# Kernel optimization log

Measured on AMD Instinct MI355X. Metric: run time of the kernel, lower is better.

## Reference

```python
import jax, jax.numpy as jnp
import numpy as np

POS_THRESH = 0.5

def cxcy_to_xy(cxcy):
    return jnp.concatenate([cxcy[..., :2] - cxcy[..., 2:] / 2,
                            cxcy[..., :2] + cxcy[..., 2:] / 2], axis=-1)

def xy_to_cxcy(xy):
    return jnp.concatenate([(xy[..., :2] + xy[..., 2:]) / 2,
                            xy[..., 2:] - xy[..., :2]], axis=-1)

def iou_matrix(a, b):
    # a: [A,4] corner boxes, b: [N,4] corner boxes -> [A,N]
    lt = jnp.maximum(a[:, None, :2], b[None, :, :2])
    rb = jnp.minimum(a[:, None, 2:], b[None, :, 2:])
    wh = jnp.clip(rb - lt, 0.0)
    inter = wh[..., 0] * wh[..., 1]
    area_a = (a[:, 2] - a[:, 0]) * (a[:, 3] - a[:, 1])
    area_b = (b[:, 2] - b[:, 0]) * (b[:, 3] - b[:, 1])
    return inter / (area_a[:, None] + area_b[None, :] - inter)

def encode(gt_cxcy, anc_cxcy):
    # standard SSD variance encoding
    g_cxcy = (gt_cxcy[:, :2] - anc_cxcy[:, :2]) / (anc_cxcy[:, 2:] / 10.0)
    g_wh = jnp.log(gt_cxcy[:, 2:] / anc_cxcy[:, 2:]) * 5.0
    return jnp.concatenate([g_cxcy, g_wh], axis=1)

def setup_inputs() -> dict:
    key = jax.random.key(0)
    k1, k2, k3, k4, k5 = jax.random.split(key, 5)
    B, N, A = 64, 64, 24564
    # valid gt corner boxes in [0,1]
    gc = jax.random.uniform(k1, (B, N, 2), minval=0.2, maxval=0.8)
    gwh = jax.random.uniform(k2, (B, N, 2), minval=0.05, maxval=0.3)
    gt_boxes = jnp.concatenate([gc - gwh / 2, gc + gwh / 2], axis=-1)
    gt_labels = jax.random.randint(k3, (B, N), 0, 20)
    ac = jax.random.uniform(k4, (A, 2), minval=0.05, maxval=0.95)
    awh = jax.random.uniform(k5, (A, 2), minval=0.03, maxval=0.5)
    center_anchor = jnp.concatenate([ac, awh], axis=-1)
    return {"gt_boxes": gt_boxes, "gt_labels": gt_labels, "center_anchor": center_anchor}

def _match_one(boxes, labels, center_anchor, corner_anchor):
    # boxes:[N,4] corner, labels:[N], anchors:[A,4]
    N = boxes.shape[0]
    iou = iou_matrix(corner_anchor, boxes)            # [A,N]
    obj_idx = jnp.argmax(iou, axis=0)                 # best anchor per object [N]
    iou = iou.at[obj_idx, jnp.arange(N)].set(1.0)     # force-match
    positive = jnp.any(iou >= POS_THRESH, axis=1)     # [A] bool
    max_anchors_idx = jnp.argmax(iou, axis=1)         # best object per anchor [A]
    classes = (labels[max_anchors_idx] + 1) * positive.astype(labels.dtype)
    gt_center = xy_to_cxcy(boxes[max_anchors_idx])    # [A,4]
    locations = encode(gt_center, center_anchor)      # [A,4]
    return classes, locations, positive

def reference(gt_boxes, gt_labels, center_anchor):
    corner_anchor = cxcy_to_xy(center_anchor)
    gt_classes, gt_locations, gt_masks = jax.vmap(
        lambda b, l: _match_one(b, l, center_anchor, corner_anchor)
    )(gt_boxes, gt_labels)
    return gt_classes, gt_locations, gt_masks
```

## Files before the change

### kernel.cpp

```cpp
#include <hip/hip_runtime.h>
#include <hip/hip_bf16.h>


#define NOBJ 64
#define TILE 512
#define SPLIT 2

__global__ void k_init(unsigned long long* __restrict__ ws, int n) {
    int i = blockIdx.x * blockDim.x + threadIdx.x;
    if (i < n) ws[i] = 0ull;
}

__global__ __launch_bounds__(256) void k_best_anchor(
    const float4* __restrict__ gt_boxes,
    const float4* __restrict__ center_anchor,
    unsigned long long* __restrict__ ws,
    int A, int N)
{
#pragma clang fp contract(off)
    __shared__ float4 sc[TILE];
    __shared__ float  sa[TILE];
    const int b    = blockIdx.y;
    const int og   = blockIdx.x >> 1;
    const int half = blockIdx.x & 1;
    const int tid  = threadIdx.x;
    const int wv   = tid >> 6;
    const int lane = tid & 63;
    const int n    = og * 4 + wv;

    const int HALF = (A + SPLIT - 1) / SPLIT;
    const int beg  = half * HALF;
    const int end  = min(A, beg + HALF);

    const float4 box  = gt_boxes[b * N + n];
    const float barea = (box.z - box.x) * (box.w - box.y);

    float best_v = -1.0f;
    int   best_i = 0;

    for (int base = beg; base < end; base += TILE) {
        const int tn = min(TILE, end - base);
        __syncthreads();
        for (int j = tid; j < tn; j += 256) {
            float4 ca = center_anchor[base + j];
            float hw = ca.z * 0.5f, hh = ca.w * 0.5f;
            float ax0 = ca.x - hw, ay0 = ca.y - hh;
            float ax1 = ca.x + hw, ay1 = ca.y + hh;
            sc[j] = make_float4(ax0, ay0, ax1, ay1);
            sa[j] = (ax1 - ax0) * (ay1 - ay0);
        }
        __syncthreads();
        for (int j = lane; j < tn; j += 64) {
            float4 c = sc[j];
            float aarea = sa[j];
            float ltx = fmaxf(c.x, box.x), lty = fmaxf(c.y, box.y);
            float rbx = fminf(c.z, box.z), rby = fminf(c.w, box.w);
            float wx = fmaxf(rbx - ltx, 0.0f), wy = fmaxf(rby - lty, 0.0f);
            float inter = wx * wy;
            float v = inter / ((aarea + barea) - inter);
            if (v > best_v) { best_v = v; best_i = base + j; }
        }
    }
    for (int m = 1; m < 64; m <<= 1) {
        float ov = __shfl_xor(best_v, m);
        int   oi = __shfl_xor(best_i, m);
        if (ov > best_v || (ov == best_v && oi < best_i)) { best_v = ov; best_i = oi; }
    }
    if (lane == 0) {
        unsigned long long key =
            ((unsigned long long)__float_as_uint(best_v) << 32) |
            (unsigned long long)(unsigned)(~(unsigned)best_i);
        atomicMax(&ws[b * N + n], key);
    }
}

__global__ __launch_bounds__(256) void k_match(
    const float4* __restrict__ gt_boxes,
    const int*    __restrict__ gt_labels,
    const float4* __restrict__ center_anchor,
    const unsigned long long* __restrict__ ws,
    float* __restrict__ out,
    int A, int N, int BA)
{
#pragma clang fp contract(off)
    __shared__ float4 sbox[NOBJ];
    __shared__ float  sbar[NOBJ];
    __shared__ int    slab[NOBJ];
    __shared__ int    sidx[NOBJ];
    const int b   = blockIdx.y;
    const int tid = threadIdx.x;
    if (tid < NOBJ) {
        float4 bx = gt_boxes[b * N + tid];
        sbox[tid] = bx;
        sbar[tid] = (bx.z - bx.x) * (bx.w - bx.y);
        slab[tid] = gt_labels[b * N + tid];
        sidx[tid] = (int)(~(unsigned)(ws[b * N + tid] & 0xffffffffull));
    }
    __syncthreads();

    const int a = blockIdx.x * 256 + tid;
    if (a >= A) return;

    const float4 ca = center_anchor[a];
    const float hw = ca.z * 0.5f, hh = ca.w * 0.5f;
    const float ax0 = ca.x - hw, ay0 = ca.y - hh;
    const float ax1 = ca.x + hw, ay1 = ca.y + hh;
    const float aarea = (ax1 - ax0) * (ay1 - ay0);

    float best_v = -1.0f;
    int   best_n = 0;

#pragma unroll 8
    for (int nn = 0; nn < NOBJ; ++nn) {
        float4 bx = sbox[nn];
        float ltx = fmaxf(ax0, bx.x), lty = fmaxf(ay0, bx.y);
        float rbx = fminf(ax1, bx.z), rby = fminf(ay1, bx.w);
        float wx = fmaxf(rbx - ltx, 0.0f), wy = fmaxf(rby - lty, 0.0f);
        float inter = wx * wy;
        float v = inter / ((aarea + sbar[nn]) - inter);
        if (sidx[nn] == a) v = 1.0f;
        if (v > best_v) { best_v = v; best_n = nn; }
    }
    const bool pos = (best_v >= 0.5f);
    const int  cls = pos ? (slab[best_n] + 1) : 0;

    const float4 gb = sbox[best_n];
    const float gcx = (gb.x + gb.z) * 0.5f;
    const float gcy = (gb.y + gb.w) * 0.5f;
    const float gw  = gb.z - gb.x;
    const float gh  = gb.w - gb.y;
    const float l0 = (gcx - ca.x) / (ca.z / 10.0f);
    const float l1 = (gcy - ca.y) / (ca.w / 10.0f);
    const float l2 = __logf(gw / ca.z) * 5.0f;
    const float l3 = __logf(gh / ca.w) * 5.0f;

    const int idx = b * A + a;
    out[idx] = (float)cls;
    reinterpret_cast<float4*>(out + (size_t)BA)[idx] =
        make_float4(l0, l1, l2, l3);
    out[(size_t)5 * BA + idx] = pos ? 1.0f : 0.0f;
}

extern "C" void kernel_launch(void* const* d_in, const int* in_sizes, int n_in,
                              void* d_out, int out_size, void* d_ws, size_t ws_size,
                              hipStream_t stream) {
    const float4* gt_boxes      = (const float4*)d_in[0];
    const int*    gt_labels     = (const int*)d_in[1];
    const float4* center_anchor = (const float4*)d_in[2];

    const int N  = NOBJ;
    const int BN = in_sizes[1];
    const int B  = BN / N;
    const int A  = in_sizes[2] / 4;
    const int BA = B * A;

    float* out = (float*)d_out;
    unsigned long long* ws = (unsigned long long*)d_ws;

    k_init<<<(BN + 255) / 256, 256, 0, stream>>>(ws, BN);

    dim3 g1((N / 4) * SPLIT, B);
    k_best_anchor<<<g1, 256, 0, stream>>>(gt_boxes, center_anchor, ws, A, N);

    dim3 g2((A + 255) / 256, B);
    k_match<<<g2, 256, 0, stream>>>(gt_boxes, gt_labels, center_anchor, ws,
                                    out, A, N, BA);
}
```

Baseline: 228.5 us.

## Process two objects per wave without LDS tiling and read match data via scalar loads

The best-anchor kernel drops its shared-memory anchor tile and barriers. Each wave now reads anchors straight from global memory and scores two objects at once, with the anchor range split four ways. Box areas are precomputed in the init kernel. The match kernel reads boxes, areas and forced-match indices per object from global memory with uniform addresses, likely scalar or cached loads, instead of staging them in shared memory. This removes syncthreads and LDS traffic but relies on the cache for the repeated anchor reads and the per-iteration global loads.

After: 224.8 us. No clear change (-1.6%).

```diff
diff --git a/kernel.cpp b/kernel.cpp
--- a/kernel.cpp
+++ b/kernel.cpp
@@ -3,74 +3,86 @@
 
 
 #define NOBJ 64
-#define TILE 512
-#define SPLIT 2
+#define SPLITK 4
 
-__global__ void k_init(unsigned long long* __restrict__ ws, int n) {
+__global__ void k_init(const float4* __restrict__ gt_boxes,
+                       unsigned long long* __restrict__ keys,
+                       float* __restrict__ areas, int BN) {
+#pragma clang fp contract(off)
     int i = blockIdx.x * blockDim.x + threadIdx.x;
-    if (i < n) ws[i] = 0ull;
+    if (i < BN) {
+        keys[i] = 0ull;
+        float4 bx = gt_boxes[i];
+        areas[i] = (bx.z - bx.x) * (bx.w - bx.y);
+    }
 }
 
 __global__ __launch_bounds__(256) void k_best_anchor(
     const float4* __restrict__ gt_boxes,
     const float4* __restrict__ center_anchor,
-    unsigned long long* __restrict__ ws,
+    unsigned long long* __restrict__ keys,
     int A, int N)
 {
 #pragma clang fp contract(off)
-    __shared__ float4 sc[TILE];
-    __shared__ float  sa[TILE];
     const int b    = blockIdx.y;
-    const int og   = blockIdx.x >> 1;
-    const int half = blockIdx.x & 1;
-    const int tid  = threadIdx.x;
-    const int wv   = tid >> 6;
-    const int lane = tid & 63;
-    const int n    = og * 4 + wv;
+    const int wv   = threadIdx.x >> 6;
+    const int lane = threadIdx.x & 63;
+    const int job  = blockIdx.x * 4 + wv;
+    const int pair = job >> 2;
+    const int spl  = job & (SPLITK - 1);
+    const int n0   = pair * 2, n1 = n0 + 1;
 
-    const int HALF = (A + SPLIT - 1) / SPLIT;
-    const int beg  = half * HALF;
-    const int end  = min(A, beg + HALF);
+    const int Q   = (A + SPLITK - 1) / SPLITK;
+    const int beg = spl * Q;
+    const int end = min(A, beg + Q);
 
-    const float4 box  = gt_boxes[b * N + n];
-    const float barea = (box.z - box.x) * (box.w - box.y);
+    const float4 B0 = gt_boxes[b * N + n0];
+    const float4 B1 = gt_boxes[b * N + n1];
+    const float ar0 = (B0.z - B0.x) * (B0.w - B0.y);
+    const float ar1 = (B1.z - B1.x) * (B1.w - B1.y);
 
-    float best_v = -1.0f;
-    int   best_i = 0;
+    float bv0 = -1.0f, bv1 = -1.0f;
+    int   bi0 = 0,     bi1 = 0;
 
-    for (int base = beg; base < end; base += TILE) {
-        const int tn = min(TILE, end - base);
-        __syncthreads();
-        for (int j = tid; j < tn; j += 256) {
-            float4 ca = center_anchor[base + j];
-            float hw = ca.z * 0.5f, hh = ca.w * 0.5f;
-            float ax0 = ca.x - hw, ay0 = ca.y - hh;
-            float ax1 = ca.x + hw, ay1 = ca.y + hh;
-            sc[j] = make_float4(ax0, ay0, ax1, ay1);
-            sa[j] = (ax1 - ax0) * (ay1 - ay0);
-        }
-        __syncthreads();
-        for (int j = lane; j < tn; j += 64) {
-            float4 c = sc[j];
-            float aarea = sa[j];
-            float ltx = fmaxf(c.x, box.x), lty = fmaxf(c.y, box.y);
-            float rbx = fminf(c.z, box.z), rby = fminf(c.w, box.w);
+    for (int j = beg + lane; j < end; j += 64) {
+        float4 ca = center_anchor[j];
+        float hw = ca.z * 0.5f, hh = ca.w * 0.5f;
+        float ax0 = ca.x - hw, ay0 = ca.y - hh;
+        float ax1 = ca.x + hw, ay1 = ca.y + hh;
+        float aarea = (ax1 - ax0) * (ay1 - ay0);
+
+        {
+            float ltx = fmaxf(ax0, B0.x), lty = fmaxf(ay0, B0.y);
+            float rbx = fminf(ax1, B0.z), rby = fminf(ay1, B0.w);
             float wx = fmaxf(rbx - ltx, 0.0f), wy = fmaxf(rby - lty, 0.0f);
             float inter = wx * wy;
-            float v = inter / ((aarea + barea) - inter);
-            if (v > best_v) { best_v = v; best_i = base + j; }
+            float v = inter / ((aarea + ar0) - inter);
+            if (v > bv0) { bv0 = v; bi0 = j; }
+        }
+        {
+            float ltx = fmaxf(ax0, B1.x), lty = fmaxf(ay0, B1.y);
+            float rbx = fminf(ax1, B1.z), rby = fminf(ay1, B1.w);
+            float wx = fmaxf(rbx - ltx, 0.0f), wy = fmaxf(rby - lty, 0.0f);
+            float inter = wx * wy;
+            float v = inter / ((aarea + ar1) - inter);
+            if (v > bv1) { bv1 = v; bi1 = j; }
         }
     }
     for (int m = 1; m < 64; m <<= 1) {
-        float ov = __shfl_xor(best_v, m);
-        int   oi = __shfl_xor(best_i, m);
-        if (ov > best_v || (ov == best_v && oi < best_i)) { best_v = ov; best_i = oi; }
+        float ov0 = __shfl_xor(bv0, m); int oi0 = __shfl_xor(bi0, m);
+        float ov1 = __shfl_xor(bv1, m); int oi1 = __shfl_xor(bi1, m);
+        if (ov0 > bv0 || (ov0 == bv0 && oi0 < bi0)) { bv0 = ov0; bi0 = oi0; }
+        if (ov1 > bv1 || (ov1 == bv1 && oi1 < bi1)) { bv1 = ov1; bi1 = oi1; }
     }
     if (lane == 0) {
-        unsigned long long key =
-            ((unsigned long long)__float_as_uint(best_v) << 32) |
-            (unsigned long long)(unsigned)(~(unsigned)best_i);
-        atomicMax(&ws[b * N + n], key);
+        unsigned long long k0 =
+            ((unsigned long long)__float_as_uint(bv0) << 32) |
+            (unsigned long long)(unsigned)(~(unsigned)bi0);
+        unsigned long long k1 =
+            ((unsigned long long)__float_as_uint(bv1) << 32) |
+            (unsigned long long)(unsigned)(~(unsigned)bi1);
+        atomicMax(&keys[b * N + n0], k0);
+        atomicMax(&keys[b * N + n1], k1);
     }
 }
 
@@ -78,23 +90,20 @@
     const float4* __restrict__ gt_boxes,
     const int*    __restrict__ gt_labels,
     const float4* __restrict__ center_anchor,
-    const unsigned long long* __restrict__ ws,
+    const unsigned long long* __restrict__ keys,
+    const float*  __restrict__ areas,
     float* __restrict__ out,
     int A, int N, int BA)
 {
 #pragma clang fp contract(off)
     __shared__ float4 sbox[NOBJ];
-    __shared__ float  sbar[NOBJ];
     __shared__ int    slab[NOBJ];
-    __shared__ int    sidx[NOBJ];
     const int b   = blockIdx.y;
     const int tid = threadIdx.x;
+    const int bN  = b * N;
     if (tid < NOBJ) {
-        float4 bx = gt_boxes[b * N + tid];
-        sbox[tid] = bx;
-        sbar[tid] = (bx.z - bx.x) * (bx.w - bx.y);
-        slab[tid] = gt_labels[b * N + tid];
-        sidx[tid] = (int)(~(unsigned)(ws[b * N + tid] & 0xffffffffull));
+        sbox[tid] = gt_boxes[bN + tid];
+        slab[tid] = gt_labels[bN + tid];
     }
     __syncthreads();
 
@@ -112,13 +121,15 @@
 
 #pragma unroll 8
     for (int nn = 0; nn < NOBJ; ++nn) {
-        float4 bx = sbox[nn];
+        const float4 bx  = gt_boxes[bN + nn];
+        const float  bar = areas[bN + nn];
+        const int    fid = (int)(~(unsigned)(keys[bN + nn] & 0xffffffffull));
         float ltx = fmaxf(ax0, bx.x), lty = fmaxf(ay0, bx.y);
         float rbx = fminf(ax1, bx.z), rby = fminf(ay1, bx.w);
         float wx = fmaxf(rbx - ltx, 0.0f), wy = fmaxf(rby - lty, 0.0f);
         float inter = wx * wy;
-        float v = inter / ((aarea + sbar[nn]) - inter);
-        if (sidx[nn] == a) v = 1.0f;
+        float v = inter / ((aarea + bar) - inter);
+        if (fid == a) v = 1.0f;
         if (v > best_v) { best_v = v; best_n = nn; }
     }
     const bool pos = (best_v >= 0.5f);
@@ -155,14 +166,15 @@
     const int BA = B * A;
 
     float* out = (float*)d_out;
-    unsigned long long* ws = (unsigned long long*)d_ws;
+    unsigned long long* keys = (unsigned long long*)d_ws;
+    float* areas = (float*)((char*)d_ws + (size_t)BN * 8);
 
-    k_init<<<(BN + 255) / 256, 256, 0, stream>>>(ws, BN);
+    k_init<<<(BN + 255) / 256, 256, 0, stream>>>(gt_boxes, keys, areas, BN);
 
-    dim3 g1((N / 4) * SPLIT, B);
-    k_best_anchor<<<g1, 256, 0, stream>>>(gt_boxes, center_anchor, ws, A, N);
+    dim3 g1((N / 2) * SPLITK / 4, B);
+    k_best_anchor<<<g1, 256, 0, stream>>>(gt_boxes, center_anchor, keys, A, N);
 
     dim3 g2((A + 255) / 256, B);
-    k_match<<<g2, 256, 0, stream>>>(gt_boxes, gt_labels, center_anchor, ws,
-                                    out, A, N, BA);
+    k_match<<<g2, 256, 0, stream>>>(gt_boxes, gt_labels, center_anchor, keys,
+                                    areas, out, A, N, BA);
 }
```

## Compute IoU matrix once, deriving per-object and per-anchor argmax in one pass

Applied to the files above, without the earlier changes.

The kernel used to compute the full anchor-object IoU matrix twice: once to find the best anchor per object and again to find the best object per anchor. It now computes it once in an anchor-parallel kernel. Each thread keeps its per-anchor best in registers and writes it to workspace. Per-object maxima are reduced across the wave with DPP and merged with 64-bit atomicMax. The final kernel only reads the stored per-anchor best and applies the force-match override with tie-handling logic. This costs an extra B*A*8-byte workspace round trip and many more atomics (one per wave per object).

Result: faster. 195.9 us (-14.3%).

```diff
diff --git a/kernel.cpp b/kernel.cpp
--- a/kernel.cpp
+++ b/kernel.cpp
@@ -1,130 +1,146 @@
 #include <hip/hip_runtime.h>
-#include <hip/hip_bf16.h>
 
 
 #define NOBJ 64
-#define TILE 512
-#define SPLIT 2
+#define VEC 4
+#define FSENT 64
 
-__global__ void k_init(unsigned long long* __restrict__ ws, int n) {
-    int i = blockIdx.x * blockDim.x + threadIdx.x;
-    if (i < n) ws[i] = 0ull;
+#define DPP0(x, ctrl) __builtin_amdgcn_update_dpp(0, (x), (ctrl), 0xF, 0xF, true)
+
+__device__ __forceinline__ float wave_max_f(float x) {
+    x = fmaxf(x, __int_as_float(DPP0(__float_as_int(x), 0x111)));
+    x = fmaxf(x, __int_as_float(DPP0(__float_as_int(x), 0x112)));
+    x = fmaxf(x, __int_as_float(DPP0(__float_as_int(x), 0x114)));
+    x = fmaxf(x, __int_as_float(DPP0(__float_as_int(x), 0x118)));
+    x = fmaxf(x, __int_as_float(DPP0(__float_as_int(x), 0x142)));
+    x = fmaxf(x, __int_as_float(DPP0(__float_as_int(x), 0x143)));
+    return x;
+}
+__device__ __forceinline__ unsigned wave_max_u(unsigned x) {
+    x = max(x, (unsigned)DPP0((int)x, 0x111));
+    x = max(x, (unsigned)DPP0((int)x, 0x112));
+    x = max(x, (unsigned)DPP0((int)x, 0x114));
+    x = max(x, (unsigned)DPP0((int)x, 0x118));
+    x = max(x, (unsigned)DPP0((int)x, 0x142));
+    x = max(x, (unsigned)DPP0((int)x, 0x143));
+    return x;
 }
 
-__global__ __launch_bounds__(256) void k_best_anchor(
+__global__ void k_init(unsigned long long* __restrict__ keys, int BN) {
+    int i = blockIdx.x * blockDim.x + threadIdx.x;
+    if (i < BN) keys[i] = 0ull;
+}
+
+__global__ __launch_bounds__(256) void k_iou(
     const float4* __restrict__ gt_boxes,
     const float4* __restrict__ center_anchor,
-    unsigned long long* __restrict__ ws,
+    unsigned long long* __restrict__ keys,
+    unsigned long long* __restrict__ pbest,
     int A, int N)
 {
 #pragma clang fp contract(off)
-    __shared__ float4 sc[TILE];
-    __shared__ float  sa[TILE];
-    const int b    = blockIdx.y;
-    const int og   = blockIdx.x >> 1;
-    const int half = blockIdx.x & 1;
-    const int tid  = threadIdx.x;
-    const int wv   = tid >> 6;
-    const int lane = tid & 63;
-    const int n    = og * 4 + wv;
+    const int b     = blockIdx.y;
+    const int wv    = threadIdx.x >> 6;
+    const int lane  = threadIdx.x & 63;
+    const int wbase = (blockIdx.x * 4 + wv) * (64 * VEC);
+    const int bN    = b * N;
 
-    const int HALF = (A + SPLIT - 1) / SPLIT;
-    const int beg  = half * HALF;
-    const int end  = min(A, beg + HALF);
+    float ax0[VEC], ay0[VEC], ax1[VEC], ay1[VEC], aar[VEC];
+    int   aidx[VEC];
+#pragma unroll
+    for (int v = 0; v < VEC; ++v) {
+        int a = wbase + v * 64 + lane;
+        if (a >= A) a = A - 1;
+        aidx[v] = a;
+        float4 ca = center_anchor[a];
+        float hw = ca.z * 0.5f, hh = ca.w * 0.5f;
+        ax0[v] = ca.x - hw; ay0[v] = ca.y - hh;
+        ax1[v] = ca.x + hw; ay1[v] = ca.y + hh;
+        aar[v] = (ax1[v] - ax0[v]) * (ay1[v] - ay0[v]);
+    }
+    float bv[VEC]; int bn[VEC];
+#pragma unroll
+    for (int v = 0; v < VEC; ++v) { bv[v] = -1.0f; bn[v] = 0; }
 
-    const float4 box  = gt_boxes[b * N + n];
-    const float barea = (box.z - box.x) * (box.w - box.y);
-
-    float best_v = -1.0f;
-    int   best_i = 0;
-
-    for (int base = beg; base < end; base += TILE) {
-        const int tn = min(TILE, end - base);
-        __syncthreads();
-        for (int j = tid; j < tn; j += 256) {
-            float4 ca = center_anchor[base + j];
-            float hw = ca.z * 0.5f, hh = ca.w * 0.5f;
-            float ax0 = ca.x - hw, ay0 = ca.y - hh;
-            float ax1 = ca.x + hw, ay1 = ca.y + hh;
-            sc[j] = make_float4(ax0, ay0, ax1, ay1);
-            sa[j] = (ax1 - ax0) * (ay1 - ay0);
-        }
-        __syncthreads();
-        for (int j = lane; j < tn; j += 64) {
-            float4 c = sc[j];
-            float aarea = sa[j];
-            float ltx = fmaxf(c.x, box.x), lty = fmaxf(c.y, box.y);
-            float rbx = fminf(c.z, box.z), rby = fminf(c.w, box.w);
+    for (int n = 0; n < NOBJ; ++n) {
+        const float4 bx  = gt_boxes[bN + n];
+        const float  bar = (bx.z - bx.x) * (bx.w - bx.y);
+        float mv = -1.0f; int ma = 0;
+#pragma unroll
+        for (int v = 0; v < VEC; ++v) {
+            float ltx = fmaxf(ax0[v], bx.x), lty = fmaxf(ay0[v], bx.y);
+            float rbx = fminf(ax1[v], bx.z), rby = fminf(ay1[v], bx.w);
             float wx = fmaxf(rbx - ltx, 0.0f), wy = fmaxf(rby - lty, 0.0f);
             float inter = wx * wy;
-            float v = inter / ((aarea + barea) - inter);
-            if (v > best_v) { best_v = v; best_i = base + j; }
+            float iou = inter / ((aar[v] + bar) - inter);
+            if (iou > bv[v]) { bv[v] = iou; bn[v] = n; }
+            if (iou > mv)    { mv = iou;    ma = aidx[v]; }
         }
+        float r = wave_max_f(mv);
+        unsigned wmb = (unsigned)__builtin_amdgcn_readlane(__float_as_int(r), 63);
+        float wmax = __uint_as_float(wmb);
+        unsigned c = (mv == wmax) ? ~(unsigned)ma : 0u;
+        c = wave_max_u(c);
+        unsigned wc = (unsigned)__builtin_amdgcn_readlane((int)c, 63);
+        if (lane == 0)
+            atomicMax(&keys[bN + n], ((unsigned long long)wmb << 32) | wc);
     }
-    for (int m = 1; m < 64; m <<= 1) {
-        float ov = __shfl_xor(best_v, m);
-        int   oi = __shfl_xor(best_i, m);
-        if (ov > best_v || (ov == best_v && oi < best_i)) { best_v = ov; best_i = oi; }
-    }
-    if (lane == 0) {
-        unsigned long long key =
-            ((unsigned long long)__float_as_uint(best_v) << 32) |
-            (unsigned long long)(unsigned)(~(unsigned)best_i);
-        atomicMax(&ws[b * N + n], key);
+    const size_t base = (size_t)b * A;
+#pragma unroll
+    for (int v = 0; v < VEC; ++v) {
+        pbest[base + aidx[v]] =
+            ((unsigned long long)__float_as_uint(bv[v]) << 32) |
+            (unsigned long long)(unsigned)bn[v];
     }
 }
 
-__global__ __launch_bounds__(256) void k_match(
+__global__ __launch_bounds__(256) void k_final(
     const float4* __restrict__ gt_boxes,
     const int*    __restrict__ gt_labels,
     const float4* __restrict__ center_anchor,
-    const unsigned long long* __restrict__ ws,
-    float* __restrict__ out,
-    int A, int N, int BA)
+    const unsigned long long* __restrict__ keys,
+    const unsigned long long* __restrict__ pbest,
+    float* __restrict__ out, int A, int N, int BA)
 {
 #pragma clang fp contract(off)
     __shared__ float4 sbox[NOBJ];
-    __shared__ float  sbar[NOBJ];
     __shared__ int    slab[NOBJ];
-    __shared__ int    sidx[NOBJ];
-    const int b   = blockIdx.y;
-    const int tid = threadIdx.x;
+    __shared__ int    sfo[NOBJ];
+    const int b = blockIdx.y, tid = threadIdx.x, bN = b * N;
     if (tid < NOBJ) {
-        float4 bx = gt_boxes[b * N + tid];
-        sbox[tid] = bx;
-        sbar[tid] = (bx.z - bx.x) * (bx.w - bx.y);
-        slab[tid] = gt_labels[b * N + tid];
-        sidx[tid] = (int)(~(unsigned)(ws[b * N + tid] & 0xffffffffull));
+        sbox[tid] = gt_boxes[bN + tid];
+        slab[tid] = gt_labels[bN + tid];
+        sfo[tid]  = (int)(~(unsigned)(keys[bN + tid] & 0xffffffffull));
     }
     __syncthreads();
 
     const int a = blockIdx.x * 256 + tid;
     if (a >= A) return;
+    const size_t ia = (size_t)b * A + a;
+
+    const unsigned long long pb = pbest[ia];
+    const float bvv = __uint_as_float((unsigned)(pb >> 32));
+    const int   bnn = (int)(pb & 0xffffffffull);
+
+    int fid = FSENT;
+#pragma unroll
+    for (int n = 0; n < NOBJ; ++n) {
+        int cn = (sfo[n] == a) ? n : FSENT;
+        fid = min(fid, cn);
+    }
+
+    bool pos; int best;
+    if (fid != FSENT) {
+        pos  = true;
+        best = (bvv == 1.0f && bnn < fid) ? bnn : fid;
+    } else {
+        pos  = (bvv >= 0.5f);
+        best = bnn;
+    }
+    const int cls = pos ? (slab[best] + 1) : 0;
 
     const float4 ca = center_anchor[a];
-    const float hw = ca.z * 0.5f, hh = ca.w * 0.5f;
-    const float ax0 = ca.x - hw, ay0 = ca.y - hh;
-    const float ax1 = ca.x + hw, ay1 = ca.y + hh;
-    const float aarea = (ax1 - ax0) * (ay1 - ay0);
-
-    float best_v = -1.0f;
-    int   best_n = 0;
-
-#pragma unroll 8
-    for (int nn = 0; nn < NOBJ; ++nn) {
-        float4 bx = sbox[nn];
-        float ltx = fmaxf(ax0, bx.x), lty = fmaxf(ay0, bx.y);
-        float rbx = fminf(ax1, bx.z), rby = fminf(ay1, bx.w);
-        float wx = fmaxf(rbx - ltx, 0.0f), wy = fmaxf(rby - lty, 0.0f);
-        float inter = wx * wy;
-        float v = inter / ((aarea + sbar[nn]) - inter);
-        if (sidx[nn] == a) v = 1.0f;
-        if (v > best_v) { best_v = v; best_n = nn; }
-    }
-    const bool pos = (best_v >= 0.5f);
-    const int  cls = pos ? (slab[best_n] + 1) : 0;
-
-    const float4 gb = sbox[best_n];
+    const float4 gb = sbox[best];
     const float gcx = (gb.x + gb.z) * 0.5f;
     const float gcy = (gb.y + gb.w) * 0.5f;
     const float gw  = gb.z - gb.x;
@@ -153,16 +169,19 @@
     const int B  = BN / N;
     const int A  = in_sizes[2] / 4;
     const int BA = B * A;
+    float* out = (float*)d_out;
 
-    float* out = (float*)d_out;
-    unsigned long long* ws = (unsigned long long*)d_ws;
+    char* w = (char*)d_ws;
+    unsigned long long* keys  = (unsigned long long*)w;
+    unsigned long long* pbest = (unsigned long long*)(w + (size_t)BN * 8);
 
-    k_init<<<(BN + 255) / 256, 256, 0, stream>>>(ws, BN);
+    k_init<<<(BN + 255) / 256, 256, 0, stream>>>(keys, BN);
 
-    dim3 g1((N / 4) * SPLIT, B);
-    k_best_anchor<<<g1, 256, 0, stream>>>(gt_boxes, center_anchor, ws, A, N);
+    const int APB = 4 * 64 * VEC;
+    dim3 g1((A + APB - 1) / APB, B);
+    k_iou<<<g1, 256, 0, stream>>>(gt_boxes, center_anchor, keys, pbest, A, N);
 
     dim3 g2((A + 255) / 256, B);
-    k_match<<<g2, 256, 0, stream>>>(gt_boxes, gt_labels, center_anchor, ws,
-                                    out, A, N, BA);
+    k_final<<<g2, 256, 0, stream>>>(gt_boxes, gt_labels, center_anchor,
+                                    keys, pbest, out, A, N, BA);
 }
```
